# Optimization experiments

Hardware: AMD Instinct MI355X
Metric: run time of the kernel (lower is better)

The kernel has to match this reference:

```python
import jax, jax.numpy as jnp
import numpy as np

CHUNK = 2048  # mirrors torch.chunk(pc, len(pc)//2048) with N a multiple of 2048


def _half(src, ref):
    """Faithful to the original: for each chunk of `src`, compute the
    [M, chunk] squared-distance matrix against `ref` and take min over the
    chunk axis (dim 1), yielding an M-vector per chunk; concatenate.
    Result shape: [num_chunks * M]."""
    chunks = src.reshape(-1, CHUNK, src.shape[-1])  # [num_chunks, CHUNK, 3]

    def per_chunk(chunk):
        diff = ref[:, None, :] - chunk[None, :, :]          # [M, CHUNK, 3]
        d = jnp.square(jnp.sqrt(jnp.sum(diff * diff, -1)))  # norm(...)**2
        return jnp.min(d, axis=1)                           # [M]

    return jax.lax.map(per_chunk, chunks).reshape(-1)


def setup_inputs() -> dict:
    key = jax.random.key(0)
    k1, k2 = jax.random.split(key)
    output_pc = jax.random.normal(k1, (1, 16384, 3), dtype=jnp.float32)
    gt_pc = jax.random.normal(k2, (1, 16384, 3), dtype=jnp.float32)
    return {"output_pc": output_pc, "gt_pc": gt_pc}


def reference(output_pc, gt_pc):
    pc1 = jnp.squeeze(output_pc)  # [N, 3]
    pc2 = jnp.squeeze(gt_pc)      # [M, 3]
    dist1 = _half(pc1, pc2)       # [ (N//CHUNK) * M ]
    dist2 = _half(pc2, pc1)       # [ (M//CHUNK) * N ]
    return jnp.mean(dist1) + jnp.mean(dist2)
```

## Files before the change

kernel.cpp:

```cpp
#include <hip/hip_runtime.h>
#include <float.h>

#define CHUNK 2048
#define SUB   512
#define MBLK  128

typedef __attribute__((ext_vector_type(8)))  short short8;
typedef __attribute__((ext_vector_type(16))) float f32x16;

static __device__ __forceinline__ unsigned short f2bf(float f) {
    unsigned u = __float_as_uint(f);
    return (unsigned short)((u + 0x7FFFu + ((u >> 16) & 1u)) >> 16);
}
static __device__ __forceinline__ float bf2f(unsigned short s) {
    return __uint_as_float(((unsigned)s) << 16);
}

__global__ void pack_kernel(const float* __restrict__ p1,
                            const float* __restrict__ p2, int n1, int n2,
                            unsigned short* __restrict__ Arec,
                            unsigned short* __restrict__ Brec)
{
    int i = blockIdx.x * blockDim.x + threadIdx.x;
    if (i >= n1 + n2) return;
    const bool isA = (i < n1);
    const float* s = isA ? p1 : p2;
    const int j = isA ? i : i - n1;
    float x = s[3 * j + 0], y = s[3 * j + 1], z = s[3 * j + 2];

    unsigned short r[16];
    if (isA) {
        unsigned short hx = f2bf(x), hy = f2bf(y), hz = f2bf(z);
        unsigned short lx = f2bf(x - bf2f(hx)), ly = f2bf(y - bf2f(hy)),
                       lz = f2bf(z - bf2f(hz));
        float sp = fmaf(x, x, fmaf(y, y, z * z));
        unsigned short sh = f2bf(sp), sl = f2bf(sp - bf2f(sh));
        r[0]=hx; r[1]=hy; r[2]=hz;  r[3]=lx; r[4]=ly; r[5]=lz;
        r[6]=hx; r[7]=hy; r[8]=hz;  r[9]=lx; r[10]=ly; r[11]=lz;
        r[12]=sh; r[13]=sl; r[14]=0x3F80; r[15]=0x3F80;
        unsigned short* dst = Arec + (size_t)j * 16;
#pragma unroll
        for (int t = 0; t < 16; ++t) dst[t] = r[t];
    } else {
        float ux = -2.0f * x, uy = -2.0f * y, uz = -2.0f * z;
        unsigned short hx = f2bf(ux), hy = f2bf(uy), hz = f2bf(uz);
        unsigned short lx = f2bf(ux - bf2f(hx)), ly = f2bf(uy - bf2f(hy)),
                       lz = f2bf(uz - bf2f(hz));
        float sq = fmaf(x, x, fmaf(y, y, z * z));
        unsigned short sh = f2bf(sq), sl = f2bf(sq - bf2f(sh));
        r[0]=hx; r[1]=hy; r[2]=hz;  r[3]=hx; r[4]=hy; r[5]=hz;
        r[6]=lx; r[7]=ly; r[8]=lz;  r[9]=lx; r[10]=ly; r[11]=lz;
        r[12]=0x3F80; r[13]=0x3F80; r[14]=sh; r[15]=sl;
        unsigned short* dst = Brec + (size_t)j * 16;
#pragma unroll
        for (int t = 0; t < 16; ++t) dst[t] = r[t];
    }
}

__global__ __launch_bounds__(256, 4)
void chamfer_mfma(const unsigned short* __restrict__ Arec,
                  const unsigned short* __restrict__ Brec,
                  float* __restrict__ colpart, float* __restrict__ rowpart,
                  int n1, int n2)
{
    __shared__ float colminW[4 * SUB];

    const int tid  = threadIdx.x;
    const int g    = blockIdx.x;
    const int yb   = blockIdx.y;
    const int lane = tid & 63;
    const int w    = tid >> 6;
    const int half = lane >> 5;
    const int l31  = lane & 31;

    const int colbase = yb * SUB;

    const int rA = g * MBLK + w * 32 + l31;
    short8 aA = *(const short8*)(Arec + (size_t)rA * 16 + half * 8);

    const unsigned short* bp =
        Brec + (size_t)(colbase + l31) * 16 + half * 8;

    const f32x16 z16 = {0,0,0,0, 0,0,0,0, 0,0,0,0, 0,0,0,0};
    float rm[16];
#pragma unroll
    for (int r = 0; r < 16; ++r) rm[r] = FLT_MAX;

#pragma unroll 2
    for (int t = 0; t < SUB / 32; ++t) {
        short8 b = *(const short8*)(bp + (size_t)t * 512);
        f32x16 d = __builtin_amdgcn_mfma_f32_32x32x16_bf16(aA, b, z16, 0, 0, 0);
#pragma unroll
        for (int r = 0; r < 16; ++r) rm[r] = fminf(rm[r], d[r]);
        float c01 = fminf(fminf(d[0], d[1]),  fminf(d[2], d[3]));
        float c23 = fminf(fminf(d[4], d[5]),  fminf(d[6], d[7]));
        float c45 = fminf(fminf(d[8], d[9]),  fminf(d[10], d[11]));
        float c67 = fminf(fminf(d[12], d[13]), fminf(d[14], d[15]));
        float cm  = fminf(fminf(c01, c23), fminf(c45, c67));
        cm = fminf(cm, __shfl_xor(cm, 32));
        cm = fmaxf(cm, 0.0f);
        if (half == 0) colminW[w * SUB + t * 32 + l31] = cm;
    }

#pragma unroll
    for (int r = 0; r < 8; ++r) {
        float lo = fminf(rm[r],     __shfl_xor(rm[r],     16));
        float hi = fminf(rm[r + 8], __shfl_xor(rm[r + 8], 16));
        rm[r] = (l31 & 16) ? hi : lo;
    }
#pragma unroll
    for (int r = 0; r < 4; ++r) {
        float lo = fminf(rm[r],     __shfl_xor(rm[r],     8));
        float hi = fminf(rm[r + 4], __shfl_xor(rm[r + 4], 8));
        rm[r] = (l31 & 8) ? hi : lo;
    }
#pragma unroll
    for (int r = 0; r < 2; ++r) {
        float lo = fminf(rm[r],     __shfl_xor(rm[r],     4));
        float hi = fminf(rm[r + 2], __shfl_xor(rm[r + 2], 4));
        rm[r] = (l31 & 4) ? hi : lo;
    }
    {
        float lo = fminf(rm[0], __shfl_xor(rm[0], 2));
        float hi = fminf(rm[1], __shfl_xor(rm[1], 2));
        rm[0] = (l31 & 2) ? hi : lo;
    }
    float v = fminf(rm[0], __shfl_xor(rm[0], 1));
    if ((l31 & 1) == 0) {
        int r = (l31 >> 1) & 15;
        int rowl = (r & 3) + 8 * (r >> 2) + 4 * half;
        int grow = g * MBLK + w * 32 + rowl;
        rowpart[(size_t)yb * n1 + grow] = fmaxf(v, 0.0f);
    }

    __syncthreads();
    for (int cb = tid; cb < SUB; cb += 256) {
        float m = fminf(fminf(colminW[0 * SUB + cb], colminW[1 * SUB + cb]),
                        fminf(colminW[2 * SUB + cb], colminW[3 * SUB + cb]));
        colpart[(size_t)g * n2 + colbase + cb] = m;
    }
}

__global__ __launch_bounds__(256)
void pass2_kernel(const float* __restrict__ colpart,
                  const float* __restrict__ rowpart, float* __restrict__ out,
                  int n1, int n2, int total1, int total2, float s1, float s2)
{
    __shared__ float wred[4];
    const int n = total1 + total2;
    float s = 0.0f;
    for (int idx = blockIdx.x * 256 + threadIdx.x; idx < n;
         idx += gridDim.x * 256) {
        float m = FLT_MAX;
        if (idx < total1) {
            int c1  = idx / n2;
            int col = idx - c1 * n2;
#pragma unroll
            for (int t = 0; t < CHUNK / MBLK; ++t)
                m = fminf(m, colpart[(size_t)(c1 * (CHUNK / MBLK) + t) * n2 + col]);
            s += fmaxf(m, 0.0f) * s1;
        } else {
            int i2  = idx - total1;
            int cc  = i2 / n1;
            int row = i2 - cc * n1;
#pragma unroll
            for (int t = 0; t < CHUNK / SUB; ++t)
                m = fminf(m, rowpart[(size_t)(cc * (CHUNK / SUB) + t) * n1 + row]);
            s += fmaxf(m, 0.0f) * s2;
        }
    }
#pragma unroll
    for (int off = 32; off > 0; off >>= 1) s += __shfl_down(s, off);
    const int lane = threadIdx.x & 63, w = threadIdx.x >> 6;
    if (lane == 0) wred[w] = s;
    __syncthreads();
    if (threadIdx.x == 0)
        atomicAdd(out, wred[0] + wred[1] + wred[2] + wred[3]);
}

#define FB_RPT  2
#define FB_TILE (256 * FB_RPT)
__global__ __launch_bounds__(256, 2)
void chamfer_valu(const float* __restrict__ p1, const float* __restrict__ p2,
                  int n1, int n2, float* __restrict__ out)
{
    __shared__ float4 q[CHUNK];
    __shared__ float wsum[4];
    const int dir = blockIdx.z;
    const float* __restrict__ src = dir ? p2 : p1;
    const float* __restrict__ ref = dir ? p1 : p2;
    const int nsrc = dir ? n2 : n1;
    const int m    = dir ? n1 : n2;
    const int nchunks = nsrc / CHUNK;
    const int c = blockIdx.y;
    const int tile0 = blockIdx.x * FB_TILE;
    if (c >= nchunks || tile0 >= m) return;
    const float scale = 1.0f / ((float)nchunks * (float)m);
    const float* __restrict__ chunk = src + (size_t)c * CHUNK * 3;
    for (int k = threadIdx.x; k < CHUNK; k += 256) {
        float x = chunk[3*k], y = chunk[3*k+1], z = chunk[3*k+2];
        q[k] = make_float4(x, y, z, fmaf(x, x, fmaf(y, y, z * z)));
    }
    __syncthreads();
    float px[FB_RPT], py[FB_RPT], pz[FB_RPT], sp[FB_RPT], mna[FB_RPT], mnb[FB_RPT];
    bool valid[FB_RPT];
#pragma unroll
    for (int r = 0; r < FB_RPT; ++r) {
        int j = tile0 + threadIdx.x + r * 256;
        valid[r] = (j < m);
        int jj = valid[r] ? j : 0;
        float x = ref[3*jj], y = ref[3*jj+1], z = ref[3*jj+2];
        px[r] = -2.0f*x; py[r] = -2.0f*y; pz[r] = -2.0f*z;
        sp[r] = fmaf(x, x, fmaf(y, y, z * z));
        mna[r] = FLT_MAX; mnb[r] = FLT_MAX;
    }
#pragma unroll 2
    for (int k = 0; k < CHUNK; k += 2) {
        float4 qa = q[k], qb = q[k+1];
#pragma unroll
        for (int r = 0; r < FB_RPT; ++r) {
            mna[r] = fminf(mna[r], fmaf(px[r], qa.x, fmaf(py[r], qa.y, fmaf(pz[r], qa.z, qa.w))));
            mnb[r] = fminf(mnb[r], fmaf(px[r], qb.x, fmaf(py[r], qb.y, fmaf(pz[r], qb.z, qb.w))));
        }
    }
    float sum = 0.0f;
#pragma unroll
    for (int r = 0; r < FB_RPT; ++r)
        if (valid[r]) sum += fmaxf(fminf(mna[r], mnb[r]) + sp[r], 0.0f);
#pragma unroll
    for (int off = 32; off > 0; off >>= 1) sum += __shfl_down(sum, off);
    if ((threadIdx.x & 63) == 0) wsum[threadIdx.x >> 6] = sum;
    __syncthreads();
    if (threadIdx.x == 0)
        atomicAdd(out, (wsum[0]+wsum[1]+wsum[2]+wsum[3]) * scale);
}

extern "C" void kernel_launch(void* const* d_in, const int* in_sizes, int n_in,
                              void* d_out, int out_size, void* d_ws, size_t ws_size,
                              hipStream_t stream)
{
    const float* p1 = (const float*)d_in[0];
    const float* p2 = (const float*)d_in[1];
    float* out = (float*)d_out;
    const int n1 = in_sizes[0] / 3;
    const int n2 = in_sizes[1] / 3;

    const int nc1 = n1 / CHUNK, nc2 = n2 / CHUNK;
    const int ng  = n1 / MBLK;
    const int nyb = n2 / SUB;

    unsigned short* Arec = (unsigned short*)d_ws;
    unsigned short* Brec = Arec + (size_t)n1 * 16;
    float* colpart = (float*)(Brec + (size_t)n2 * 16);
    float* rowpart = colpart + (size_t)ng * n2;
    const size_t need = (size_t)n1 * 32 + (size_t)n2 * 32 +
                        ((size_t)ng * n2 + (size_t)nyb * n1) * 4;

    const bool shapes_ok = (n1 % CHUNK == 0) && (n2 % CHUNK == 0) &&
                           (n1 % MBLK == 0) && (n2 % SUB == 0);

    if (shapes_ok && ws_size >= need) {
        pack_kernel<<<(n1 + n2 + 255) / 256, 256, 0, stream>>>(
            p1, p2, n1, n2, Arec, Brec);
        dim3 grid(ng, nyb);
        chamfer_mfma<<<grid, 256, 0, stream>>>(Arec, Brec, colpart, rowpart, n1, n2);
        const int total1 = nc1 * n2, total2 = nc2 * n1;
        pass2_kernel<<<512, 256, 0, stream>>>(
            colpart, rowpart, out, n1, n2, total1, total2,
            1.0f / ((float)nc1 * (float)n2), 1.0f / ((float)nc2 * (float)n1));
    } else {
        const int t1 = (n2 + FB_TILE - 1) / FB_TILE;
        const int t2 = (n1 + FB_TILE - 1) / FB_TILE;
        dim3 grid(max(t1, t2), max(nc1, nc2), 2);
        chamfer_valu<<<grid, 256, 0, stream>>>(p1, p2, n1, n2, out);
    }
}
```

Before: 96.25 us.

## Compute each chamfer direction separately instead of fusing column reductions

The MFMA kernel gains a second grid dimension for direction and computes only row minima, with operand roles swapped for the reverse direction. This replaces the per-tile column-min reduction, its LDS buffer and barrier, and the large 128-way column-partial array with a 4-way partial for each direction. The cost is twice as many MFMA tiles, in exchange for less VALU work per tile and less partial-buffer memory traffic. It also prefetches the next B fragment inside the loop and raises the occupancy hint in launch bounds.

```diff
diff --git a/kernel.cpp b/kernel.cpp
--- a/kernel.cpp
+++ b/kernel.cpp
@@ -57,49 +57,48 @@
     }
 }
 
-__global__ __launch_bounds__(256, 4)
+__global__ __launch_bounds__(256, 8)
 void chamfer_mfma(const unsigned short* __restrict__ Arec,
                   const unsigned short* __restrict__ Brec,
-                  float* __restrict__ colpart, float* __restrict__ rowpart,
+                  float* __restrict__ part2, float* __restrict__ part1,
                   int n1, int n2)
 {
-    __shared__ float colminW[4 * SUB];
+    const int dir = blockIdx.z;
+    const unsigned short* __restrict__ Ap = dir ? Brec : Arec;
+    const unsigned short* __restrict__ Bp = dir ? Arec : Brec;
+    float* __restrict__ part = dir ? part1 : part2;
+    const int rows_n = dir ? n2 : n1;
+    const int cols_n = dir ? n1 : n2;
 
     const int tid  = threadIdx.x;
     const int g    = blockIdx.x;
     const int yb   = blockIdx.y;
+    if (g * MBLK >= rows_n || yb * SUB >= cols_n) return;
+
     const int lane = tid & 63;
     const int w    = tid >> 6;
     const int half = lane >> 5;
     const int l31  = lane & 31;
 
-    const int colbase = yb * SUB;
-
     const int rA = g * MBLK + w * 32 + l31;
-    short8 aA = *(const short8*)(Arec + (size_t)rA * 16 + half * 8);
+    short8 aA = *(const short8*)(Ap + (size_t)rA * 16 + half * 8);
 
     const unsigned short* bp =
-        Brec + (size_t)(colbase + l31) * 16 + half * 8;
+        Bp + (size_t)(yb * SUB + l31) * 16 + half * 8;
 
     const f32x16 z16 = {0,0,0,0, 0,0,0,0, 0,0,0,0, 0,0,0,0};
     float rm[16];
 #pragma unroll
     for (int r = 0; r < 16; ++r) rm[r] = FLT_MAX;
 
-#pragma unroll 2
+    short8 b = *(const short8*)bp;
     for (int t = 0; t < SUB / 32; ++t) {
-        short8 b = *(const short8*)(bp + (size_t)t * 512);
+        const int tn = (t + 1 < SUB / 32) ? t + 1 : t;
+        short8 bn = *(const short8*)(bp + (size_t)tn * 512);
         f32x16 d = __builtin_amdgcn_mfma_f32_32x32x16_bf16(aA, b, z16, 0, 0, 0);
 #pragma unroll
         for (int r = 0; r < 16; ++r) rm[r] = fminf(rm[r], d[r]);
-        float c01 = fminf(fminf(d[0], d[1]),  fminf(d[2], d[3]));
-        float c23 = fminf(fminf(d[4], d[5]),  fminf(d[6], d[7]));
-        float c45 = fminf(fminf(d[8], d[9]),  fminf(d[10], d[11]));
-        float c67 = fminf(fminf(d[12], d[13]), fminf(d[14], d[15]));
-        float cm  = fminf(fminf(c01, c23), fminf(c45, c67));
-        cm = fminf(cm, __shfl_xor(cm, 32));
-        cm = fmaxf(cm, 0.0f);
-        if (half == 0) colminW[w * SUB + t * 32 + l31] = cm;
+        b = bn;
     }
 
 #pragma unroll
@@ -130,43 +129,37 @@
         int r = (l31 >> 1) & 15;
         int rowl = (r & 3) + 8 * (r >> 2) + 4 * half;
         int grow = g * MBLK + w * 32 + rowl;
-        rowpart[(size_t)yb * n1 + grow] = fmaxf(v, 0.0f);
-    }
-
-    __syncthreads();
-    for (int cb = tid; cb < SUB; cb += 256) {
-        float m = fminf(fminf(colminW[0 * SUB + cb], colminW[1 * SUB + cb]),
-                        fminf(colminW[2 * SUB + cb], colminW[3 * SUB + cb]));
-        colpart[(size_t)g * n2 + colbase + cb] = m;
+        part[(size_t)yb * rows_n + grow] = fmaxf(v, 0.0f);
     }
 }
 
 __global__ __launch_bounds__(256)
-void pass2_kernel(const float* __restrict__ colpart,
-                  const float* __restrict__ rowpart, float* __restrict__ out,
-                  int n1, int n2, int total1, int total2, float s1, float s2)
+void pass2_kernel(const float* __restrict__ part2,
+                  const float* __restrict__ part1, float* __restrict__ out,
+                  int n1, int n2, int total2, int total1, float s2, float s1)
 {
     __shared__ float wred[4];
-    const int n = total1 + total2;
+    const int gpc = CHUNK / SUB;
+    const int n = total2 + total1;
     float s = 0.0f;
     for (int idx = blockIdx.x * 256 + threadIdx.x; idx < n;
          idx += gridDim.x * 256) {
         float m = FLT_MAX;
-        if (idx < total1) {
-            int c1  = idx / n2;
-            int col = idx - c1 * n2;
-#pragma unroll
-            for (int t = 0; t < CHUNK / MBLK; ++t)
-                m = fminf(m, colpart[(size_t)(c1 * (CHUNK / MBLK) + t) * n2 + col]);
+        if (idx < total2) {
+            int cc  = idx / n1;
+            int row = idx - cc * n1;
+#pragma unroll
+            for (int t = 0; t < gpc; ++t)
+                m = fminf(m, part2[(size_t)(cc * gpc + t) * n1 + row]);
+            s += fmaxf(m, 0.0f) * s2;
+        } else {
+            int i1  = idx - total2;
+            int c1  = i1 / n2;
+            int col = i1 - c1 * n2;
+#pragma unroll
+            for (int t = 0; t < gpc; ++t)
+                m = fminf(m, part1[(size_t)(c1 * gpc + t) * n2 + col]);
             s += fmaxf(m, 0.0f) * s1;
-        } else {
-            int i2  = idx - total1;
-            int cc  = i2 / n1;
-            int row = i2 - cc * n1;
-#pragma unroll
-            for (int t = 0; t < CHUNK / SUB; ++t)
-                m = fminf(m, rowpart[(size_t)(cc * (CHUNK / SUB) + t) * n1 + row]);
-            s += fmaxf(m, 0.0f) * s2;
         }
     }
 #pragma unroll
@@ -246,28 +239,31 @@
     const int n2 = in_sizes[1] / 3;
 
     const int nc1 = n1 / CHUNK, nc2 = n2 / CHUNK;
-    const int ng  = n1 / MBLK;
-    const int nyb = n2 / SUB;
+    const int nyb2 = n2 / SUB;
+    const int nyb1 = n1 / SUB;
 
     unsigned short* Arec = (unsigned short*)d_ws;
     unsigned short* Brec = Arec + (size_t)n1 * 16;
-    float* colpart = (float*)(Brec + (size_t)n2 * 16);
-    float* rowpart = colpart + (size_t)ng * n2;
+    float* part2 = (float*)(Brec + (size_t)n2 * 16);
+    float* part1 = part2 + (size_t)nyb2 * n1;
     const size_t need = (size_t)n1 * 32 + (size_t)n2 * 32 +
-                        ((size_t)ng * n2 + (size_t)nyb * n1) * 4;
+                        ((size_t)nyb2 * n1 + (size_t)nyb1 * n2) * 4;
 
     const bool shapes_ok = (n1 % CHUNK == 0) && (n2 % CHUNK == 0) &&
-                           (n1 % MBLK == 0) && (n2 % SUB == 0);
+                           (n1 % MBLK == 0) && (n2 % MBLK == 0) &&
+                           (n1 % SUB == 0) && (n2 % SUB == 0);
 
     if (shapes_ok && ws_size >= need) {
         pack_kernel<<<(n1 + n2 + 255) / 256, 256, 0, stream>>>(
             p1, p2, n1, n2, Arec, Brec);
-        dim3 grid(ng, nyb);
-        chamfer_mfma<<<grid, 256, 0, stream>>>(Arec, Brec, colpart, rowpart, n1, n2);
-        const int total1 = nc1 * n2, total2 = nc2 * n1;
+        const int gx = max(n1, n2) / MBLK;
+        const int gy = max(n1, n2) / SUB;
+        dim3 grid(gx, gy, 2);
+        chamfer_mfma<<<grid, 256, 0, stream>>>(Arec, Brec, part2, part1, n1, n2);
+        const int total2 = nc2 * n1, total1 = nc1 * n2;
         pass2_kernel<<<512, 256, 0, stream>>>(
-            colpart, rowpart, out, n1, n2, total1, total2,
-            1.0f / ((float)nc1 * (float)n2), 1.0f / ((float)nc2 * (float)n1));
+            part2, part1, out, n1, n2, total2, total1,
+            1.0f / ((float)nc2 * (float)n1), 1.0f / ((float)nc1 * (float)n2));
     } else {
         const int t1 = (n2 + FB_TILE - 1) / FB_TILE;
         const int t2 = (n1 + FB_TILE - 1) / FB_TILE;
```

Result: faster. 91.42 us (-5.0%).
